# Kernel tuning notes

Hardware: AMD Instinct MI355X
Metric: run time of the kernel (lower is better)

The kernel has to match this reference:

```python
import jax, jax.numpy as jnp
import numpy as np


def setup_inputs() -> dict:
    key = jax.random.key(0)
    k_y, k_cb = jax.random.split(key)
    B, C, H, W = 8, 192, 64, 64
    G, K = 8, 512
    d = C // G  # 24
    y = jax.random.normal(k_y, (B, C, H, W), dtype=jnp.float32)
    codebooks = jax.random.normal(k_cb, (G, K, d), dtype=jnp.float32)
    return {"y": y, "codebooks": codebooks}


def reference(y, codebooks):
    # y: [B, C, H, W]; codebooks: [G, K, d] with C == G*d
    B, C, H, W = y.shape
    G, K, d = codebooks.shape
    # split channels into G groups of dim d -> vectors at each spatial pos
    x = y.reshape(B, G, d, H, W).transpose(0, 3, 4, 1, 2)  # [B,H,W,G,d]
    x2 = jnp.sum(x * x, axis=-1, keepdims=True)            # [B,H,W,G,1]
    e2 = jnp.sum(codebooks * codebooks, axis=-1)           # [G,K]
    xe = jnp.einsum('bhwgd,gkd->bhwgk', x, codebooks)      # [B,H,W,G,K]
    dist = x2 - 2.0 * xe + e2                              # [B,H,W,G,K]
    idx = jnp.argmin(dist, axis=-1)                        # [B,H,W,G] int
    # gather quantized vectors per group (to_feather)
    q = codebooks[jnp.arange(G), idx]                      # [B,H,W,G,d]
    y_ba = q.transpose(0, 3, 4, 1, 2).reshape(B, C, H, W)  # [B,C,H,W]
    code_index = idx.transpose(0, 3, 1, 2)                 # [B,G,H,W]
    # straight-through estimator
    universal_ctx = y + jax.lax.stop_gradient(y_ba - y)
    return universal_ctx, y_ba, code_index[:, None]        # [B,1,G,H,W]
```

## Files before the change

kernel.cpp:

```cpp
#include <hip/hip_runtime.h>

#define B_   8
#define C_   192
#define HW_  4096
#define G_   8
#define K_   512
#define D_   24
#define CBSZ (K_ * D_)
#define THREADS 256
#define TILES_PER_BLOCK 8

typedef float  f32x4 __attribute__((ext_vector_type(4)));
typedef int    i32x4 __attribute__((ext_vector_type(4)));
typedef short  s16x8 __attribute__((ext_vector_type(8)));
typedef short  s16x4 __attribute__((ext_vector_type(4)));
typedef unsigned long long u64;

static __device__ __forceinline__ unsigned umin_(unsigned a, unsigned b){return a<b?a:b;}
static __device__ __forceinline__ unsigned umax_(unsigned a, unsigned b){return a>b?a:b;}
static __device__ __forceinline__ unsigned short f2bf(float x){
    unsigned u=__float_as_uint(x);
    return (unsigned short)((u + 0x7FFFu + ((u>>16)&1u))>>16);
}
static __device__ __forceinline__ float bf2f(unsigned short h){return __uint_as_float(((unsigned)h)<<16);}

__global__ __launch_bounds__(THREADS) void vq_stage(
    const float* __restrict__ cb, unsigned short* __restrict__ ws)
{
    const int g = blockIdx.x >> 3;
    const int s = blockIdx.x & 7;
    const int tid = threadIdx.x;
    const float* cbg = cb + g * CBSZ;
    unsigned short* img = ws + g * 16384;

    for (int i = tid; i < 384; i += THREADS) {
        int gi = s * 384 + i;
        f32x4 v = ((const f32x4*)cbg)[gi];
        int i4 = gi << 2;
        int n  = i4 / 24;
        int k0 = i4 - n * 24;
        int off = (n >> 4) * 512 + (((k0 >> 3) << 4) + (n & 15)) * 8 + (k0 & 7);
        s16x4 h;
        h[0]=(short)f2bf(v[0]); h[1]=(short)f2bf(v[1]);
        h[2]=(short)f2bf(v[2]); h[3]=(short)f2bf(v[3]);
        *(s16x4*)(&img[off]) = h;
    }
    if (tid < 64) {
        int n = s * 64 + tid;
        const float* row = cbg + n * D_;
        double s0 = 0.0, s1 = 0.0;
        #pragma unroll
        for (int j = 0; j < D_; j += 2) {
            double v0 = (double)row[j], v1 = (double)row[j+1];
            s0 = fma(v0,v0,s0); s1 = fma(v1,v1,s1);
        }
        double sv = s0 + s1;
        unsigned short ehi = f2bf((float)sv);
        unsigned short elo = f2bf((float)(sv - (double)bf2f(ehi)));
        i32x4 pack = { (int)((unsigned)ehi | ((unsigned)elo << 16)), 0, 0, 0 };
        *(i32x4*)(&img[(n >> 4) * 512 + (48 + (n & 15)) * 8]) = pack;
    }
}

__global__ __launch_bounds__(THREADS, 5) void vq_mfma5(
    const float* __restrict__ y, const float* __restrict__ cb,
    const unsigned short* __restrict__ ws, float* __restrict__ out)
{
    __shared__ unsigned short sB[32 * 512];

    const int bid = blockIdx.x;
    const int g = bid & 7;
    const int chunk = bid >> 3;
    const int tid = threadIdx.x;
    const int wave = tid >> 6, lane = tid & 63;
    const int c = lane & 15, q = lane >> 4;

    const float* cbg = cb + g * CBSZ;

    {
        const char* src = (const char*)(ws + g * 16384);
        char* dst = (char*)sB;
        #pragma unroll
        for (int it = 0; it < 8; ++it)
            *(i32x4*)(dst + it*4096 + tid*16) = *(const i32x4*)(src + it*4096 + tid*16);
    }
    __syncthreads();

    float* out0 = out;
    float* out1 = out + B_*C_*HW_;
    float* out2 = out + 2*B_*C_*HW_;

    for (int mt = wave; mt < TILES_PER_BLOCK; mt += 4) {
        const int posT = chunk * (TILES_PER_BLOCK*16) + mt * 16;
        const int bimg = posT >> 12;
        const int hw   = posT & (HW_-1);
        const int ybase = (bimg*C_ + g*D_)*HW_ + hw;
        const float* yb = y + ybase;

        float xf[8];
        unsigned hx[4], lx[4];
        if (q < 3) {
            const float* yq = yb + (q*8)*HW_ + c;
            #pragma unroll
            for (int jj = 0; jj < 8; ++jj) xf[jj] = -2.0f * yq[jj*HW_];
            #pragma unroll
            for (int p2 = 0; p2 < 4; ++p2) {
                float f0 = xf[2*p2], f1 = xf[2*p2+1];
                unsigned u0 = __float_as_uint(f0), u1v = __float_as_uint(f1);
                hx[p2] = (u1v & 0xFFFF0000u) | (u0 >> 16);
                float l0 = f0 - __uint_as_float(u0 & 0xFFFF0000u);
                float l1 = f1 - __uint_as_float(u1v & 0xFFFF0000u);
                lx[p2] = (unsigned)f2bf(l0) | ((unsigned)f2bf(l1) << 16);
            }
        } else {
            #pragma unroll
            for (int jj = 0; jj < 8; ++jj) xf[jj] = 0.0f;
            hx[0] = 0x3F803F80u; hx[1]=0u; hx[2]=0u; hx[3]=0u;
            lx[0]=0u; lx[1]=0u; lx[2]=0u; lx[3]=0u;
        }
        const s16x8 Xh = __builtin_bit_cast(s16x8, (i32x4){(int)hx[0],(int)hx[1],(int)hx[2],(int)hx[3]});
        const s16x8 Xl = __builtin_bit_cast(s16x8, (i32x4){(int)lx[0],(int)lx[1],(int)lx[2],(int)lx[3]});

        unsigned b1=0xFFFFFFFFu, b2=0xFFFFFFFFu, b3=0xFFFFFFFFu;
        const unsigned qr4 = (unsigned)(q << 2);
        #pragma unroll 8
        for (int t = 0; t < 32; ++t) {
            s16x8 eh = *(const s16x8*)(&sB[t*512 + lane*8]);
            f32x4 acc = {256.0f, 256.0f, 256.0f, 256.0f};
            acc = __builtin_amdgcn_mfma_f32_16x16x32_bf16(eh, Xh, acc, 0,0,0);
            acc = __builtin_amdgcn_mfma_f32_16x16x32_bf16(eh, Xl, acc, 0,0,0);
            const unsigned cbase = ((unsigned)t << 4) + qr4;
            #pragma unroll
            for (int r = 0; r < 4; ++r) {
                unsigned key = (__float_as_uint(acc[r]) & 0xFFFFFE00u) + (cbase + r);
                b3 = umin_(umax_(b2, key), b3);
                b2 = umin_(umax_(b1, key), b2);
                b1 = umin_(b1, key);
            }
        }

        #pragma unroll
        for (int d = 16; d < 64; d <<= 1) {
            unsigned o1=__shfl_xor(b1,d,64), o2=__shfl_xor(b2,d,64), o3=__shfl_xor(b3,d,64);
            unsigned x = umax_(b1,o1);
            unsigned yv= umin_(b2,o2);
            unsigned w = umax_(b2,o2);
            unsigned z = umin_(b3,o3);
            b1 = umin_(b1,o1);
            b2 = umin_(x,yv);
            b3 = umin_(umax_(x,yv), umin_(w,z));
        }

        const float v1 = __uint_as_float(b1 & 0xFFFFFE00u);
        const float v2 = __uint_as_float(b2 & 0xFFFFFE00u);
        int kwin;
        if (__ballot((v2 - v1) < 0.20f) == 0ull) {
            kwin = (int)(b1 & 511u);
        } else {
            double xd[8];
            #pragma unroll
            for (int jj = 0; jj < 8; ++jj) xd[jj] = (double)xf[jj];
            const unsigned cands[3] = {b1, b2, b3};
            u64 bestk = ~0ull;
            #pragma unroll
            for (int ci = 0; ci < 3; ++ci) {
                int kc = (int)(cands[ci] & 511u);
                double s = 0.0;
                if (q < 3) {
                    const f32x4* ce4 = (const f32x4*)(cbg + kc*D_ + (q<<3));
                    float ef[8];
                    *(f32x4*)&ef[0] = ce4[0];
                    *(f32x4*)&ef[4] = ce4[1];
                    #pragma unroll
                    for (int jj = 0; jj < 8; ++jj) {
                        double ev = (double)ef[jj];
                        s = fma(ev, ev, s);
                        s = fma(xd[jj], ev, s);
                    }
                }
                s += __shfl_xor(s, 16, 64);
                s += __shfl_xor(s, 32, 64);
                s += 256.0;
                u64 kk = (((u64)__double_as_longlong(s)) & ~0x1FFull) | (u64)kc;
                bestk = kk < bestk ? kk : bestk;
            }
            kwin = (int)(bestk & 511ull);
        }

        const float* cw = cbg + kwin * D_;
        if (q < 3) {
            const f32x4* cw4 = (const f32x4*)(cw + (q<<3));
            float v[8];
            *(f32x4*)&v[0] = cw4[0];
            *(f32x4*)&v[4] = cw4[1];
            const int ob = ybase + (q*8)*HW_ + c;
            #pragma unroll
            for (int jj = 0; jj < 8; ++jj) {
                out0[ob + jj*HW_] = v[jj];
                out1[ob + jj*HW_] = v[jj];
            }
        }
        if (lane < 16)
            out2[(bimg*G_ + g)*HW_ + hw + lane] = (float)kwin;
    }
}

extern "C" void kernel_launch(void* const* d_in, const int* in_sizes, int n_in,
                              void* d_out, int out_size, void* d_ws, size_t ws_size,
                              hipStream_t stream) {
    const float* y  = (const float*)d_in[0];
    const float* cb = (const float*)d_in[1];
    float* out = (float*)d_out;
    unsigned short* ws = (unsigned short*)d_ws;

    vq_stage<<<dim3(64), dim3(THREADS), 0, stream>>>(cb, ws);
    const int nblocks = 256 * G_;
    vq_mfma5<<<dim3(nblocks), dim3(THREADS), 0, stream>>>(y, cb, ws, out);
}
```

Baseline: 117.9 us.

## Compact codebook LDS image, load norms as accumulator init, use med3 top-3

The staged codebook image drops the per-tile bf16 norm rows and stores code norms (plus the bias 256) as a separate fp32 array, which shrinks LDS per block. The norms are now loaded straight into the MFMA accumulator, so the constant row in the X operand is no longer needed and the norm is kept in fp32 instead of a bf16 hi/lo pair. The smaller LDS footprint allows 6 blocks per CU. The grid becomes 1536 blocks that each stride over tiles, sized so every block stays resident at once. The top-3 insertion uses v_med3_u32, which cuts the ALU ops in the inner loop.

```diff
diff --git a/kernel.cpp b/kernel.cpp
--- a/kernel.cpp
+++ b/kernel.cpp
@@ -8,7 +8,12 @@
 #define D_   24
 #define CBSZ (K_ * D_)
 #define THREADS 256
-#define TILES_PER_BLOCK 8
+
+#define FRAG_HW   12288
+#define IMG_HW    13312
+#define LDS_BYTES 26624
+#define TILES_PER_GROUP 2048
+#define WAVES_PER_GROUP 768
 
 typedef float  f32x4 __attribute__((ext_vector_type(4)));
 typedef int    i32x4 __attribute__((ext_vector_type(4)));
@@ -22,7 +27,6 @@
     unsigned u=__float_as_uint(x);
     return (unsigned short)((u + 0x7FFFu + ((u>>16)&1u))>>16);
 }
-static __device__ __forceinline__ float bf2f(unsigned short h){return __uint_as_float(((unsigned)h)<<16);}
 
 __global__ __launch_bounds__(THREADS) void vq_stage(
     const float* __restrict__ cb, unsigned short* __restrict__ ws)
@@ -31,7 +35,7 @@
     const int s = blockIdx.x & 7;
     const int tid = threadIdx.x;
     const float* cbg = cb + g * CBSZ;
-    unsigned short* img = ws + g * 16384;
+    unsigned short* img = ws + g * IMG_HW;
 
     for (int i = tid; i < 384; i += THREADS) {
         int gi = s * 384 + i;
@@ -39,7 +43,7 @@
         int i4 = gi << 2;
         int n  = i4 / 24;
         int k0 = i4 - n * 24;
-        int off = (n >> 4) * 512 + (((k0 >> 3) << 4) + (n & 15)) * 8 + (k0 & 7);
+        int off = (n >> 4) * 384 + (((k0 >> 3) << 4) + (n & 15)) * 8 + (k0 & 7);
         s16x4 h;
         h[0]=(short)f2bf(v[0]); h[1]=(short)f2bf(v[1]);
         h[2]=(short)f2bf(v[2]); h[3]=(short)f2bf(v[3]);
@@ -54,23 +58,19 @@
             double v0 = (double)row[j], v1 = (double)row[j+1];
             s0 = fma(v0,v0,s0); s1 = fma(v1,v1,s1);
         }
-        double sv = s0 + s1;
-        unsigned short ehi = f2bf((float)sv);
-        unsigned short elo = f2bf((float)(sv - (double)bf2f(ehi)));
-        i32x4 pack = { (int)((unsigned)ehi | ((unsigned)elo << 16)), 0, 0, 0 };
-        *(i32x4*)(&img[(n >> 4) * 512 + (48 + (n & 15)) * 8]) = pack;
-    }
-}
-
-__global__ __launch_bounds__(THREADS, 5) void vq_mfma5(
+        ((float*)(img + FRAG_HW))[n] = (float)(256.0 + s0 + s1);
+    }
+}
+
+__global__ __launch_bounds__(THREADS, 6) void vq_mfma6(
     const float* __restrict__ y, const float* __restrict__ cb,
     const unsigned short* __restrict__ ws, float* __restrict__ out)
 {
-    __shared__ unsigned short sB[32 * 512];
+    __shared__ __align__(16) unsigned short sB[IMG_HW];
 
     const int bid = blockIdx.x;
     const int g = bid & 7;
-    const int chunk = bid >> 3;
+    const int blkg = bid >> 3;
     const int tid = threadIdx.x;
     const int wave = tid >> 6, lane = tid & 63;
     const int c = lane & 15, q = lane >> 4;
@@ -78,11 +78,14 @@
     const float* cbg = cb + g * CBSZ;
 
     {
-        const char* src = (const char*)(ws + g * 16384);
+        const char* src = (const char*)(ws + g * IMG_HW);
         char* dst = (char*)sB;
         #pragma unroll
-        for (int it = 0; it < 8; ++it)
-            *(i32x4*)(dst + it*4096 + tid*16) = *(const i32x4*)(src + it*4096 + tid*16);
+        for (int it = 0; it < 7; ++it) {
+            int off = it * 4096 + tid * 16;
+            if (off < LDS_BYTES)
+                *(i32x4*)(dst + off) = *(const i32x4*)(src + off);
+        }
     }
     __syncthreads();
 
@@ -90,10 +93,14 @@
     float* out1 = out + B_*C_*HW_;
     float* out2 = out + 2*B_*C_*HW_;
 
-    for (int mt = wave; mt < TILES_PER_BLOCK; mt += 4) {
-        const int posT = chunk * (TILES_PER_BLOCK*16) + mt * 16;
-        const int bimg = posT >> 12;
-        const int hw   = posT & (HW_-1);
+    const unsigned short* aptr = sB + (lane < 48 ? lane : lane - 48) * 8;
+    const f32x4* e2p = (const f32x4*)((const float*)(sB + FRAG_HW) + (q << 2));
+
+    const int wsid = (blkg << 2) + wave;
+
+    for (int tt = wsid; tt < TILES_PER_GROUP; tt += WAVES_PER_GROUP) {
+        const int bimg = tt >> 8;
+        const int hw   = (tt & 255) << 4;
         const int ybase = (bimg*C_ + g*D_)*HW_ + hw;
         const float* yb = y + ybase;
 
@@ -115,7 +122,7 @@
         } else {
             #pragma unroll
             for (int jj = 0; jj < 8; ++jj) xf[jj] = 0.0f;
-            hx[0] = 0x3F803F80u; hx[1]=0u; hx[2]=0u; hx[3]=0u;
+            hx[0]=0u; hx[1]=0u; hx[2]=0u; hx[3]=0u;
             lx[0]=0u; lx[1]=0u; lx[2]=0u; lx[3]=0u;
         }
         const s16x8 Xh = __builtin_bit_cast(s16x8, (i32x4){(int)hx[0],(int)hx[1],(int)hx[2],(int)hx[3]});
@@ -125,16 +132,18 @@
         const unsigned qr4 = (unsigned)(q << 2);
         #pragma unroll 8
         for (int t = 0; t < 32; ++t) {
-            s16x8 eh = *(const s16x8*)(&sB[t*512 + lane*8]);
-            f32x4 acc = {256.0f, 256.0f, 256.0f, 256.0f};
+            s16x8 eh = *(const s16x8*)(aptr + t * 384);
+            f32x4 acc = e2p[t * 4];
             acc = __builtin_amdgcn_mfma_f32_16x16x32_bf16(eh, Xh, acc, 0,0,0);
             acc = __builtin_amdgcn_mfma_f32_16x16x32_bf16(eh, Xl, acc, 0,0,0);
             const unsigned cbase = ((unsigned)t << 4) + qr4;
             #pragma unroll
             for (int r = 0; r < 4; ++r) {
                 unsigned key = (__float_as_uint(acc[r]) & 0xFFFFFE00u) + (cbase + r);
-                b3 = umin_(umax_(b2, key), b3);
-                b2 = umin_(umax_(b1, key), b2);
+                unsigned t3, t2;
+                asm("v_med3_u32 %0, %1, %2, %3" : "=v"(t3) : "v"(key), "v"(b2), "v"(b3));
+                asm("v_med3_u32 %0, %1, %2, %3" : "=v"(t2) : "v"(key), "v"(b1), "v"(b2));
+                b3 = t3; b2 = t2;
                 b1 = umin_(b1, key);
             }
         }
@@ -214,6 +223,6 @@
     unsigned short* ws = (unsigned short*)d_ws;
 
     vq_stage<<<dim3(64), dim3(THREADS), 0, stream>>>(cb, ws);
-    const int nblocks = 256 * G_;
-    vq_mfma5<<<dim3(nblocks), dim3(THREADS), 0, stream>>>(y, cb, ws, out);
-}
+    const int nblocks = 192 * G_;
+    vq_mfma6<<<dim3(nblocks), dim3(THREADS), 0, stream>>>(y, cb, ws, out);
+}
```

Measured after the change: 114.0 us. -3.2%, faster.
